# Optimization experiments

Measured on AMD Instinct MI355X. Metric: run time of the kernel, lower is better.

The kernel has to match this reference:

```python
import jax, jax.numpy as jnp
import numpy as np

N_NODES = 100000
N_EDGES = 600000
IN_FEAT = 128
OUT_FEAT = 128
NUM_RELS = 8
NUM_BASES = 4


def setup_inputs() -> dict:
    key = jax.random.key(0)
    ks = jax.random.split(key, 8)
    h = jax.random.normal(ks[0], (N_NODES, IN_FEAT), dtype=jnp.float32)
    # xavier-ish scale for params
    weight = jax.random.normal(ks[1], (NUM_BASES, IN_FEAT, OUT_FEAT), dtype=jnp.float32) * (1.0 / np.sqrt(IN_FEAT))
    w_comp = jax.random.normal(ks[2], (NUM_RELS, NUM_BASES), dtype=jnp.float32) * (1.0 / np.sqrt(NUM_BASES))
    root_weight = jax.random.normal(ks[3], (IN_FEAT, OUT_FEAT), dtype=jnp.float32) * (1.0 / np.sqrt(IN_FEAT))
    bias = jnp.zeros((OUT_FEAT,), dtype=jnp.float32)
    src = jax.random.randint(ks[4], (N_EDGES,), 0, N_NODES, dtype=jnp.int32)
    dst = jax.random.randint(ks[5], (N_EDGES,), 0, N_NODES, dtype=jnp.int32)
    rel_type = jax.random.randint(ks[6], (N_EDGES,), 0, NUM_RELS, dtype=jnp.int32)
    return {"h": h, "weight": weight, "w_comp": w_comp, "root_weight": root_weight,
            "bias": bias, "src": src, "dst": dst, "rel_type": rel_type}


def reference(h, weight, w_comp, root_weight, bias, src, dst, rel_type):
    # Basis decomposition: W[r] = sum_b w_comp[r,b] * weight[b]
    B, I, O = weight.shape
    R = w_comp.shape[0]
    W = (w_comp @ weight.reshape(B, I * O)).reshape(R, I, O)  # [R, in, out]
    # msg_e = h[src_e] @ W[rel_e]; computed as all-relation projection + gather
    # (avoids materializing [E, in, out] per-edge weights)
    proj = jnp.einsum('ni,rio->nro', h, W)          # [N, R, out]
    msg = proj[src, rel_type]                        # [E, out]
    agg = jax.ops.segment_sum(msg, dst, num_segments=h.shape[0])  # scatter-sum
    out = h @ root_weight + agg + bias
    return jax.nn.relu(out)
```

## Files before the change

### kernel.cpp

```cpp
#include <hip/hip_runtime.h>
#include <hip/hip_bf16.h>

#define N_NODES 100000
#define N_EDGES 600000
#define FEAT 128
#define NUM_RELS 8
#define NUM_BASES 4
#define NB1 391
#define NBE 2344

typedef short bf16x8 __attribute__((ext_vector_type(8)));
typedef float f32x4  __attribute__((ext_vector_type(4)));

__device__ inline short f2bf(float x) {
    __hip_bfloat16 b = __float2bfloat16(x);
    return *reinterpret_cast<short*>(&b);
}
__device__ inline float bfbits2f(unsigned int u16) {
    return __int_as_float(u16 << 16);
}
__device__ inline unsigned int fbits(float x) { return __float_as_uint(x); }


__global__ __launch_bounds__(256) void k_cast_h(const float* __restrict__ h,
                                                short* __restrict__ hb) {
    int i = blockIdx.x * 256 + threadIdx.x;
    if (i < N_NODES * FEAT / 8) {
        const float4* h4 = (const float4*)h;
        float4 v0 = h4[2 * i], v1 = h4[2 * i + 1];
        union { short s[8]; bf16x8 v; } u;
        u.s[0] = f2bf(v0.x); u.s[1] = f2bf(v0.y); u.s[2] = f2bf(v0.z); u.s[3] = f2bf(v0.w);
        u.s[4] = f2bf(v1.x); u.s[5] = f2bf(v1.y); u.s[6] = f2bf(v1.z); u.s[7] = f2bf(v1.w);
        ((bf16x8*)hb)[i] = u.v;
    }
}

__global__ __launch_bounds__(256) void k_build_b(const float* __restrict__ weight,
                                                 const float* __restrict__ rw,
                                                 short* __restrict__ Bt) {
    int idx = blockIdx.x * 256 + threadIdx.x;
    if (idx < 5 * FEAT * FEAT) {
        int kc = idx >> 14;
        int e  = idx & 16383;
        int o  = e >> 7, ip = e & 127;
        float v = (kc == 0) ? rw[ip * FEAT + o]
                            : weight[(kc - 1) * FEAT * FEAT + ip * FEAT + o];
        Bt[idx] = f2bf(v);
    }
}

__global__ __launch_bounds__(256) void k_hist_dst(const int* __restrict__ dst,
                                                  int* __restrict__ cnt) {
    int i = blockIdx.x * 256 + threadIdx.x;
    if (i < N_EDGES) atomicAdd(&cnt[dst[i]], 1);
}

__global__ __launch_bounds__(256) void k_s1(const int* __restrict__ cnt,
                                            int* __restrict__ bsum) {
    int i = blockIdx.x * 256 + threadIdx.x;
    int v = (i < N_NODES) ? cnt[i] : 0;
#pragma unroll
    for (int d = 32; d; d >>= 1) v += __shfl_down(v, d);
    __shared__ int w4[4];
    if ((threadIdx.x & 63) == 0) w4[threadIdx.x >> 6] = v;
    __syncthreads();
    if (threadIdx.x == 0) bsum[blockIdx.x] = w4[0] + w4[1] + w4[2] + w4[3];
}

__global__ void k_s2(const int* __restrict__ bsum,
                     int* __restrict__ bbase,
                     int* __restrict__ offs) {
    if (blockIdx.x == 0 && threadIdx.x == 0) {
        int acc = 0;
        for (int b = 0; b < NB1; ++b) { bbase[b] = acc; acc += bsum[b]; }
        offs[N_NODES] = acc;
    }
}

__global__ __launch_bounds__(256) void k_s3(const int* __restrict__ cnt,
                                            const int* __restrict__ bbase,
                                            int* __restrict__ offs,
                                            int* __restrict__ cursor) {
    int i = blockIdx.x * 256 + threadIdx.x;
    int lane = threadIdx.x & 63, wid = threadIdx.x >> 6;
    int v = (i < N_NODES) ? cnt[i] : 0;
    int incl = v;
#pragma unroll
    for (int d = 1; d < 64; d <<= 1) {
        int t = __shfl_up(incl, d);
        if (lane >= d) incl += t;
    }
    __shared__ int wsum[4];
    if (lane == 63) wsum[wid] = incl;
    __syncthreads();
    if (threadIdx.x == 0) {
        int a = 0;
#pragma unroll
        for (int w = 0; w < 4; ++w) { int x = wsum[w]; wsum[w] = a; a += x; }
    }
    __syncthreads();
    int ex = incl - v + wsum[wid] + bbase[blockIdx.x];
    if (i < N_NODES) { offs[i] = ex; cursor[i] = ex; }
}

__global__ __launch_bounds__(256) void k_scatter_sorted(const int* __restrict__ src,
                                                        const int* __restrict__ dst,
                                                        const int* __restrict__ rel,
                                                        const float* __restrict__ wc,
                                                        int* __restrict__ cursor,
                                                        int* __restrict__ srcs,
                                                        float4* __restrict__ coef) {
    int e = blockIdx.x * 256 + threadIdx.x;
    if (e < N_EDGES) {
        int p = atomicAdd(&cursor[dst[e]], 1);
        srcs[p] = src[e];
        int r = rel[e] * NUM_BASES;
        coef[p] = make_float4(wc[r], wc[r + 1], wc[r + 2], wc[r + 3]);
    }
}

__global__ __launch_bounds__(256) void k_edge_z(const int* __restrict__ offs,
                                                const int* __restrict__ srcs,
                                                const float4* __restrict__ coef,
                                                const short* __restrict__ hb,
                                                unsigned int* __restrict__ z_u32) {
    int wid = threadIdx.x >> 6, lane = threadIdx.x & 63;
    int d = blockIdx.x * 4 + wid;
    if (d >= N_NODES) return;
    int s = offs[d], e = offs[d + 1];

    float zx[4] = {0.f, 0.f, 0.f, 0.f};
    float zy[4] = {0.f, 0.f, 0.f, 0.f};

    int i = s;
    for (; i + 1 < e; i += 2) {
        int s0 = srcs[i], s1 = srcs[i + 1];
        float4 c0 = coef[i], c1 = coef[i + 1];
        unsigned int v0 = ((const unsigned int*)(hb + (size_t)s0 * FEAT))[lane];
        unsigned int v1 = ((const unsigned int*)(hb + (size_t)s1 * FEAT))[lane];
        float a0 = bfbits2f(v0 & 0xffffu), b0 = bfbits2f(v0 >> 16);
        float a1 = bfbits2f(v1 & 0xffffu), b1 = bfbits2f(v1 >> 16);
        zx[0] += c0.x * a0; zy[0] += c0.x * b0;
        zx[1] += c0.y * a0; zy[1] += c0.y * b0;
        zx[2] += c0.z * a0; zy[2] += c0.z * b0;
        zx[3] += c0.w * a0; zy[3] += c0.w * b0;
        zx[0] += c1.x * a1; zy[0] += c1.x * b1;
        zx[1] += c1.y * a1; zy[1] += c1.y * b1;
        zx[2] += c1.z * a1; zy[2] += c1.z * b1;
        zx[3] += c1.w * a1; zy[3] += c1.w * b1;
    }
    if (i < e) {
        int s0 = srcs[i];
        float4 c0 = coef[i];
        unsigned int v0 = ((const unsigned int*)(hb + (size_t)s0 * FEAT))[lane];
        float a0 = bfbits2f(v0 & 0xffffu), b0 = bfbits2f(v0 >> 16);
        zx[0] += c0.x * a0; zy[0] += c0.x * b0;
        zx[1] += c0.y * a0; zy[1] += c0.y * b0;
        zx[2] += c0.z * a0; zy[2] += c0.z * b0;
        zx[3] += c0.w * a0; zy[3] += c0.w * b0;
    }

    unsigned int* row = z_u32 + (size_t)d * 256;
#pragma unroll
    for (int b = 0; b < 4; ++b) {
        unsigned int lo = ((unsigned int)(unsigned short)f2bf(zx[b]));
        unsigned int hi = ((unsigned int)(unsigned short)f2bf(zy[b])) << 16;
        row[b * 64 + lane] = lo | hi;
    }
}

__global__ __launch_bounds__(256) void k_gemm_fused(const short* __restrict__ hb,
                                                    const short* __restrict__ z,
                                                    const short* __restrict__ Bt,
                                                    const float* __restrict__ bias,
                                                    float* __restrict__ out) {
    __shared__ short lds[FEAT * FEAT];
    int wave = threadIdx.x >> 6, lane = threadIdx.x & 63;
    int quad = lane >> 4, n16 = lane & 15;
    int base = blockIdx.x * 128 + wave * 32;

    int rowA0 = base + n16;        if (rowA0 >= N_NODES) rowA0 = N_NODES - 1;
    int rowA1 = base + 16 + n16;   if (rowA1 >= N_NODES) rowA1 = N_NODES - 1;

    f32x4 acc[2][8];
#pragma unroll
    for (int mt = 0; mt < 2; ++mt)
#pragma unroll
        for (int nt = 0; nt < 8; ++nt) acc[mt][nt] = (f32x4)0.f;

    float4* l4 = (float4*)lds;
    const bf16x8* bp = (const bf16x8*)lds;

    for (int kc = 0; kc < 5; ++kc) {
        if (kc) __syncthreads();
        const float4* s4 = (const float4*)(Bt + kc * FEAT * FEAT);
#pragma unroll
        for (int t = 0; t < 8; ++t) {
            int linear = threadIdx.x + t * 256;
            int o = linear >> 4, c = linear & 15;
            l4[(o << 4) + ((c + (o >> 3)) & 15)] = s4[linear];
        }
        __syncthreads();

        const bf16x8* a0p = (kc == 0)
            ? (const bf16x8*)(hb + (size_t)rowA0 * FEAT)
            : (const bf16x8*)(z + (size_t)rowA0 * 512 + (kc - 1) * FEAT);
        const bf16x8* a1p = (kc == 0)
            ? (const bf16x8*)(hb + (size_t)rowA1 * FEAT)
            : (const bf16x8*)(z + (size_t)rowA1 * 512 + (kc - 1) * FEAT);

#pragma unroll
        for (int ks = 0; ks < 4; ++ks) {
            bf16x8 a0 = a0p[ks * 4 + quad];
            bf16x8 a1 = a1p[ks * 4 + quad];
            int sw = (ks * 4 + quad + n16) & 15;
#pragma unroll
            for (int nt = 0; nt < 8; ++nt) {
                int o = n16 * 8 + nt;
                bf16x8 b = bp[(o << 4) + sw];
                acc[0][nt] = __builtin_amdgcn_mfma_f32_16x16x32_bf16(a0, b, acc[0][nt], 0, 0, 0);
                acc[1][nt] = __builtin_amdgcn_mfma_f32_16x16x32_bf16(a1, b, acc[1][nt], 0, 0, 0);
            }
        }
    }

    float bv[8];
#pragma unroll
    for (int nt = 0; nt < 8; ++nt) bv[nt] = bias[n16 * 8 + nt];

#pragma unroll
    for (int mt = 0; mt < 2; ++mt)
#pragma unroll
        for (int reg = 0; reg < 4; ++reg) {
            int node = base + mt * 16 + quad * 4 + reg;
            if (node < N_NODES) {
                float4 fa, fb;
                fa.x = fmaxf(acc[mt][0][reg] + bv[0], 0.f);
                fa.y = fmaxf(acc[mt][1][reg] + bv[1], 0.f);
                fa.z = fmaxf(acc[mt][2][reg] + bv[2], 0.f);
                fa.w = fmaxf(acc[mt][3][reg] + bv[3], 0.f);
                fb.x = fmaxf(acc[mt][4][reg] + bv[4], 0.f);
                fb.y = fmaxf(acc[mt][5][reg] + bv[5], 0.f);
                fb.z = fmaxf(acc[mt][6][reg] + bv[6], 0.f);
                fb.w = fmaxf(acc[mt][7][reg] + bv[7], 0.f);
                float* row = out + (size_t)node * FEAT + n16 * 8;
                *(float4*)row       = fa;
                *(float4*)(row + 4) = fb;
            }
        }
}


extern "C" void kernel_launch(void* const* d_in, const int* in_sizes, int n_in,
                              void* d_out, int out_size, void* d_ws, size_t ws_size,
                              hipStream_t stream) {
    const float* h    = (const float*)d_in[0];
    const float* wgt  = (const float*)d_in[1];
    const float* wcmp = (const float*)d_in[2];
    const float* rw   = (const float*)d_in[3];
    const float* bias = (const float*)d_in[4];
    const int*   src  = (const int*)d_in[5];
    const int*   dst  = (const int*)d_in[6];
    const int*   rel  = (const int*)d_in[7];
    float* out = (float*)d_out;

    char* ws = (char*)d_ws;
    short*        hb     = (short*)(ws + 0);
    short*        Bt     = (short*)(ws + 25600000ull);
    short*        z      = (short*)(ws + 25763840ull);
    unsigned int* z_u32  = (unsigned int*)z;
    int*          srcs   = (int*)(ws + 128163840ull);
    float4*       coef   = (float4*)(ws + 130563840ull);
    int*          cnt    = (int*)(ws + 140163840ull);
    int*          offs   = (int*)(ws + 140563840ull);
    int*          cursor = (int*)(ws + 140963968ull);
    int*          bsum   = (int*)(ws + 141363968ull);
    int*          bbase  = (int*)(ws + 141366016ull);

    hipLaunchKernelGGL(k_cast_h,   dim3(6250), dim3(256), 0, stream, h, hb);
    hipLaunchKernelGGL(k_build_b,  dim3(320),  dim3(256), 0, stream, wgt, rw, Bt);
    hipMemsetAsync(cnt, 0, N_NODES * sizeof(int), stream);
    hipLaunchKernelGGL(k_hist_dst, dim3(NBE),  dim3(256), 0, stream, dst, cnt);
    hipLaunchKernelGGL(k_s1,       dim3(NB1),  dim3(256), 0, stream, cnt, bsum);
    hipLaunchKernelGGL(k_s2,       dim3(1),    dim3(64),  0, stream, bsum, bbase, offs);
    hipLaunchKernelGGL(k_s3,       dim3(NB1),  dim3(256), 0, stream, cnt, bbase, offs, cursor);
    hipLaunchKernelGGL(k_scatter_sorted, dim3(NBE), dim3(256), 0, stream,
                       src, dst, rel, wcmp, cursor, srcs, coef);
    hipLaunchKernelGGL(k_edge_z,   dim3((N_NODES + 3) / 4), dim3(256), 0, stream,
                       offs, srcs, coef, hb, z_u32);
    hipLaunchKernelGGL(k_gemm_fused, dim3((N_NODES + 127) / 128), dim3(256), 0, stream,
                       hb, z, Bt, bias, out);
}
```

Baseline: 286.2 us.

## Merge prep kernels and replace three-pass scan with single-block scan

Fuses the h cast, basis-matrix build and count zeroing into one launch that branches on block index, removing a memset and a kernel launch. Replaces the three-kernel multi-block prefix sum with a single 256-thread block that walks the counts in int4 chunks and carries a running total. Also rewrites the edge accumulation with two-wide float vectors so the compiler can emit packed FMAs. The trade-off is that the scan now runs serially on one CU across roughly a hundred iterations, each with barriers, which could cost more than the launches it removes.

Result: slower. 337.8 us (+18.0%).

```diff
diff --git a/kernel.cpp b/kernel.cpp
--- a/kernel.cpp
+++ b/kernel.cpp
@@ -6,11 +6,16 @@
 #define FEAT 128
 #define NUM_RELS 8
 #define NUM_BASES 4
-#define NB1 391
 #define NBE 2344
+
+#define PREP_CAST 6250
+#define PREP_BLDB 320
+#define PREP_ZERO 391
+#define PREP_GRID (PREP_CAST + PREP_BLDB + PREP_ZERO)
 
 typedef short bf16x8 __attribute__((ext_vector_type(8)));
 typedef float f32x4  __attribute__((ext_vector_type(4)));
+typedef float f32x2  __attribute__((ext_vector_type(2)));
 
 __device__ inline short f2bf(float x) {
     __hip_bfloat16 b = __float2bfloat16(x);
@@ -19,33 +24,34 @@
 __device__ inline float bfbits2f(unsigned int u16) {
     return __int_as_float(u16 << 16);
 }
-__device__ inline unsigned int fbits(float x) { return __float_as_uint(x); }
-
-
-__global__ __launch_bounds__(256) void k_cast_h(const float* __restrict__ h,
-                                                short* __restrict__ hb) {
-    int i = blockIdx.x * 256 + threadIdx.x;
-    if (i < N_NODES * FEAT / 8) {
+
+
+__global__ __launch_bounds__(256) void k_prep(const float* __restrict__ h,
+                                              const float* __restrict__ weight,
+                                              const float* __restrict__ rw,
+                                              short* __restrict__ hb,
+                                              short* __restrict__ Bt,
+                                              int* __restrict__ cnt) {
+    int b = blockIdx.x;
+    if (b < PREP_CAST) {
+        int i = b * 256 + threadIdx.x;
         const float4* h4 = (const float4*)h;
         float4 v0 = h4[2 * i], v1 = h4[2 * i + 1];
         union { short s[8]; bf16x8 v; } u;
         u.s[0] = f2bf(v0.x); u.s[1] = f2bf(v0.y); u.s[2] = f2bf(v0.z); u.s[3] = f2bf(v0.w);
         u.s[4] = f2bf(v1.x); u.s[5] = f2bf(v1.y); u.s[6] = f2bf(v1.z); u.s[7] = f2bf(v1.w);
         ((bf16x8*)hb)[i] = u.v;
-    }
-}
-
-__global__ __launch_bounds__(256) void k_build_b(const float* __restrict__ weight,
-                                                 const float* __restrict__ rw,
-                                                 short* __restrict__ Bt) {
-    int idx = blockIdx.x * 256 + threadIdx.x;
-    if (idx < 5 * FEAT * FEAT) {
+    } else if (b < PREP_CAST + PREP_BLDB) {
+        int idx = (b - PREP_CAST) * 256 + threadIdx.x;
         int kc = idx >> 14;
         int e  = idx & 16383;
         int o  = e >> 7, ip = e & 127;
         float v = (kc == 0) ? rw[ip * FEAT + o]
                             : weight[(kc - 1) * FEAT * FEAT + ip * FEAT + o];
         Bt[idx] = f2bf(v);
+    } else {
+        int i = (b - PREP_CAST - PREP_BLDB) * 256 + threadIdx.x;
+        if (i < N_NODES) cnt[i] = 0;
     }
 }
 
@@ -55,52 +61,50 @@
     if (i < N_EDGES) atomicAdd(&cnt[dst[i]], 1);
 }
 
-__global__ __launch_bounds__(256) void k_s1(const int* __restrict__ cnt,
-                                            int* __restrict__ bsum) {
-    int i = blockIdx.x * 256 + threadIdx.x;
-    int v = (i < N_NODES) ? cnt[i] : 0;
-#pragma unroll
-    for (int d = 32; d; d >>= 1) v += __shfl_down(v, d);
-    __shared__ int w4[4];
-    if ((threadIdx.x & 63) == 0) w4[threadIdx.x >> 6] = v;
-    __syncthreads();
-    if (threadIdx.x == 0) bsum[blockIdx.x] = w4[0] + w4[1] + w4[2] + w4[3];
-}
-
-__global__ void k_s2(const int* __restrict__ bsum,
-                     int* __restrict__ bbase,
-                     int* __restrict__ offs) {
-    if (blockIdx.x == 0 && threadIdx.x == 0) {
-        int acc = 0;
-        for (int b = 0; b < NB1; ++b) { bbase[b] = acc; acc += bsum[b]; }
-        offs[N_NODES] = acc;
-    }
-}
-
-__global__ __launch_bounds__(256) void k_s3(const int* __restrict__ cnt,
-                                            const int* __restrict__ bbase,
-                                            int* __restrict__ offs,
-                                            int* __restrict__ cursor) {
-    int i = blockIdx.x * 256 + threadIdx.x;
+__global__ __launch_bounds__(256) void k_scan(const int* __restrict__ cnt,
+                                              int* __restrict__ offs,
+                                              int* __restrict__ cursor) {
+    __shared__ int wsum[4];
+    __shared__ int btot_s;
     int lane = threadIdx.x & 63, wid = threadIdx.x >> 6;
-    int v = (i < N_NODES) ? cnt[i] : 0;
-    int incl = v;
-#pragma unroll
-    for (int d = 1; d < 64; d <<= 1) {
-        int t = __shfl_up(incl, d);
-        if (lane >= d) incl += t;
-    }
-    __shared__ int wsum[4];
-    if (lane == 63) wsum[wid] = incl;
-    __syncthreads();
-    if (threadIdx.x == 0) {
-        int a = 0;
-#pragma unroll
-        for (int w = 0; w < 4; ++w) { int x = wsum[w]; wsum[w] = a; a += x; }
-    }
-    __syncthreads();
-    int ex = incl - v + wsum[wid] + bbase[blockIdx.x];
-    if (i < N_NODES) { offs[i] = ex; cursor[i] = ex; }
+    const int4* cnt4 = (const int4*)cnt;
+    int4* offs4 = (int4*)offs;
+    int4* cur4  = (int4*)cursor;
+    int carry = 0;
+    const int NIT = (N_NODES / 4 + 255) / 256;
+    for (int c = 0; c < NIT; ++c) {
+        int i4 = c * 256 + threadIdx.x;
+        int4 v = (i4 < N_NODES / 4) ? cnt4[i4] : make_int4(0, 0, 0, 0);
+        int s = v.x + v.y + v.z + v.w;
+        int incl = s;
+#pragma unroll
+        for (int d = 1; d < 64; d <<= 1) {
+            int t = __shfl_up(incl, d);
+            if (lane >= d) incl += t;
+        }
+        __syncthreads();
+        if (lane == 63) wsum[wid] = incl;
+        __syncthreads();
+        if (threadIdx.x == 0) {
+            int a = 0;
+#pragma unroll
+            for (int w = 0; w < 4; ++w) { int x = wsum[w]; wsum[w] = a; a += x; }
+            btot_s = a;
+        }
+        __syncthreads();
+        int base = incl - s + wsum[wid] + carry;
+        if (i4 < N_NODES / 4) {
+            int4 ex;
+            ex.x = base;
+            ex.y = base + v.x;
+            ex.z = base + v.x + v.y;
+            ex.w = base + v.x + v.y + v.z;
+            offs4[i4] = ex;
+            cur4[i4]  = ex;
+        }
+        carry += btot_s;
+    }
+    if (threadIdx.x == 0) offs[N_NODES] = carry;
 }
 
 __global__ __launch_bounds__(256) void k_scatter_sorted(const int* __restrict__ src,
@@ -129,8 +133,7 @@
     if (d >= N_NODES) return;
     int s = offs[d], e = offs[d + 1];
 
-    float zx[4] = {0.f, 0.f, 0.f, 0.f};
-    float zy[4] = {0.f, 0.f, 0.f, 0.f};
+    f32x2 z2[4] = {(f32x2)0.f, (f32x2)0.f, (f32x2)0.f, (f32x2)0.f};
 
     int i = s;
     for (; i + 1 < e; i += 2) {
@@ -138,33 +141,35 @@
         float4 c0 = coef[i], c1 = coef[i + 1];
         unsigned int v0 = ((const unsigned int*)(hb + (size_t)s0 * FEAT))[lane];
         unsigned int v1 = ((const unsigned int*)(hb + (size_t)s1 * FEAT))[lane];
-        float a0 = bfbits2f(v0 & 0xffffu), b0 = bfbits2f(v0 >> 16);
-        float a1 = bfbits2f(v1 & 0xffffu), b1 = bfbits2f(v1 >> 16);
-        zx[0] += c0.x * a0; zy[0] += c0.x * b0;
-        zx[1] += c0.y * a0; zy[1] += c0.y * b0;
-        zx[2] += c0.z * a0; zy[2] += c0.z * b0;
-        zx[3] += c0.w * a0; zy[3] += c0.w * b0;
-        zx[0] += c1.x * a1; zy[0] += c1.x * b1;
-        zx[1] += c1.y * a1; zy[1] += c1.y * b1;
-        zx[2] += c1.z * a1; zy[2] += c1.z * b1;
-        zx[3] += c1.w * a1; zy[3] += c1.w * b1;
+        f32x2 h0; h0.x = bfbits2f(v0 & 0xffffu); h0.y = bfbits2f(v0 >> 16);
+        f32x2 h1; h1.x = bfbits2f(v1 & 0xffffu); h1.y = bfbits2f(v1 >> 16);
+        f32x2 cc;
+        cc = c0.x; z2[0] += cc * h0;
+        cc = c0.y; z2[1] += cc * h0;
+        cc = c0.z; z2[2] += cc * h0;
+        cc = c0.w; z2[3] += cc * h0;
+        cc = c1.x; z2[0] += cc * h1;
+        cc = c1.y; z2[1] += cc * h1;
+        cc = c1.z; z2[2] += cc * h1;
+        cc = c1.w; z2[3] += cc * h1;
     }
     if (i < e) {
         int s0 = srcs[i];
         float4 c0 = coef[i];
         unsigned int v0 = ((const unsigned int*)(hb + (size_t)s0 * FEAT))[lane];
-        float a0 = bfbits2f(v0 & 0xffffu), b0 = bfbits2f(v0 >> 16);
-        zx[0] += c0.x * a0; zy[0] += c0.x * b0;
-        zx[1] += c0.y * a0; zy[1] += c0.y * b0;
-        zx[2] += c0.z * a0; zy[2] += c0.z * b0;
-        zx[3] += c0.w * a0; zy[3] += c0.w * b0;
+        f32x2 h0; h0.x = bfbits2f(v0 & 0xffffu); h0.y = bfbits2f(v0 >> 16);
+        f32x2 cc;
+        cc = c0.x; z2[0] += cc * h0;
+        cc = c0.y; z2[1] += cc * h0;
+        cc = c0.z; z2[2] += cc * h0;
+        cc = c0.w; z2[3] += cc * h0;
     }
 
     unsigned int* row = z_u32 + (size_t)d * 256;
 #pragma unroll
     for (int b = 0; b < 4; ++b) {
-        unsigned int lo = ((unsigned int)(unsigned short)f2bf(zx[b]));
-        unsigned int hi = ((unsigned int)(unsigned short)f2bf(zy[b])) << 16;
+        unsigned int lo = ((unsigned int)(unsigned short)f2bf(z2[b].x));
+        unsigned int hi = ((unsigned int)(unsigned short)f2bf(z2[b].y)) << 16;
         row[b * 64 + lane] = lo | hi;
     }
 }
@@ -274,16 +279,11 @@
     int*          cnt    = (int*)(ws + 140163840ull);
     int*          offs   = (int*)(ws + 140563840ull);
     int*          cursor = (int*)(ws + 140963968ull);
-    int*          bsum   = (int*)(ws + 141363968ull);
-    int*          bbase  = (int*)(ws + 141366016ull);
-
-    hipLaunchKernelGGL(k_cast_h,   dim3(6250), dim3(256), 0, stream, h, hb);
-    hipLaunchKernelGGL(k_build_b,  dim3(320),  dim3(256), 0, stream, wgt, rw, Bt);
-    hipMemsetAsync(cnt, 0, N_NODES * sizeof(int), stream);
+
+    hipLaunchKernelGGL(k_prep,     dim3(PREP_GRID), dim3(256), 0, stream,
+                       h, wgt, rw, hb, Bt, cnt);
     hipLaunchKernelGGL(k_hist_dst, dim3(NBE),  dim3(256), 0, stream, dst, cnt);
-    hipLaunchKernelGGL(k_s1,       dim3(NB1),  dim3(256), 0, stream, cnt, bsum);
-    hipLaunchKernelGGL(k_s2,       dim3(1),    dim3(64),  0, stream, bsum, bbase, offs);
-    hipLaunchKernelGGL(k_s3,       dim3(NB1),  dim3(256), 0, stream, cnt, bbase, offs, cursor);
+    hipLaunchKernelGGL(k_scan,     dim3(1),    dim3(256), 0, stream, cnt, offs, cursor);
     hipLaunchKernelGGL(k_scatter_sorted, dim3(NBE), dim3(256), 0, stream,
                        src, dst, rel, wcmp, cursor, srcs, coef);
     hipLaunchKernelGGL(k_edge_z,   dim3((N_NODES + 3) / 4), dim3(256), 0, stream,
```
